# Optimization experiments

Hardware: AMD Instinct MI355X
Metric: run time of the kernel (lower is better)

## Reference

```python
import jax, jax.numpy as jnp
import numpy as np

B, T, D = 4, 2048, 1024
H = 16
HD = D // H  # 64


def setup_inputs() -> dict:
    key = jax.random.key(0)
    ks = jax.random.split(key, 9)
    x = jax.random.normal(ks[0], (B, T, D), dtype=jnp.float32)
    s = 0.02
    Wq = jax.random.normal(ks[1], (D, D), dtype=jnp.float32) * s
    bq = jnp.zeros((D,), dtype=jnp.float32)
    Wk = jax.random.normal(ks[2], (D, D), dtype=jnp.float32) * s
    bk = jnp.zeros((D,), dtype=jnp.float32)
    Wv = jax.random.normal(ks[3], (D, D), dtype=jnp.float32) * s
    bv = jnp.zeros((D,), dtype=jnp.float32)
    Wo = jax.random.normal(ks[4], (D, D), dtype=jnp.float32) * s
    bo = jnp.zeros((D,), dtype=jnp.float32)
    return {"x": x, "Wq": Wq, "bq": bq, "Wk": Wk, "bk": bk,
            "Wv": Wv, "bv": bv, "Wo": Wo, "bo": bo}


def reference(x, Wq, bq, Wk, bk, Wv, bv, Wo, bo):
    Bn, Tn, Dn = x.shape
    # projections -> [B, H, T, HD]
    def split_heads(y):
        return y.reshape(Bn, Tn, H, HD).transpose(0, 2, 1, 3)
    Q = split_heads(x @ Wq + bq)
    K = split_heads(x @ Wk + bk)
    V = split_heads(x @ Wv + bv)
    scores = jnp.einsum('bhqd,bhkd->bhqk', Q, K) / jnp.sqrt(jnp.float32(HD))
    attn = jax.nn.softmax(scores, axis=-1)           # [B, H, T, T]
    attn_weights = attn.mean(axis=1)                 # [B, T, T] (head-averaged)
    out = jnp.einsum('bhqk,bhkd->bhqd', attn, V)     # [B, H, T, HD]
    out = out.transpose(0, 2, 1, 3).reshape(Bn, Tn, Dn)
    out = out @ Wo + bo                              # [B, T, D]
    # pooling weight: mean over query dim -> [B, 1, T] -> transpose -> [B, T, 1]
    pool_w = attn_weights.mean(axis=1, keepdims=True).transpose(0, 2, 1)
    pooled = (out * pool_w).sum(axis=1)              # [B, D]
    return pooled
```

## Files before the change

kernel.cpp:

```cpp
#include <hip/hip_runtime.h>
#include <hip/hip_bf16.h>
#include <stdint.h>

#define B_ 4
#define T_ 2048
#define D_ 1024
#define H_ 16
#define HD_ 64

#define QSCALE 0.1803368801111244f

typedef __bf16 bf16_t;
typedef __bf16 bf16x8 __attribute__((ext_vector_type(8)));
typedef __bf16 bf16x4 __attribute__((ext_vector_type(4)));
typedef float f32x4 __attribute__((ext_vector_type(4)));

__device__ __forceinline__ f32x4 mfma16(bf16x8 a, bf16x8 b, f32x4 c) {
  return __builtin_amdgcn_mfma_f32_16x16x32_bf16(a, b, c, 0, 0, 0);
}

__device__ __forceinline__ void gload_lds16(const bf16_t* g, bf16_t* l) {
  __builtin_amdgcn_global_load_lds(
      (const __attribute__((address_space(1))) unsigned int*)g,
      (__attribute__((address_space(3))) unsigned int*)l, 16, 0, 0);
}

__device__ __forceinline__ float exp2g(float x) {
  return __builtin_amdgcn_exp2f(x);
}

__global__ __launch_bounds__(256) void conv_x(const float* __restrict__ x,
                                              bf16_t* __restrict__ xb) {
  size_t i = ((size_t)blockIdx.x * 256 + threadIdx.x) * 8;
  float4 a = *(const float4*)(x + i);
  float4 b = *(const float4*)(x + i + 4);
  bf16x8 v;
  v[0] = (bf16_t)a.x; v[1] = (bf16_t)a.y; v[2] = (bf16_t)a.z; v[3] = (bf16_t)a.w;
  v[4] = (bf16_t)b.x; v[5] = (bf16_t)b.y; v[6] = (bf16_t)b.z; v[7] = (bf16_t)b.w;
  *(bf16x8*)(xb + i) = v;
}

__global__ __launch_bounds__(256) void conv_wt3(
    const float* __restrict__ Wq, const float* __restrict__ Wk,
    const float* __restrict__ Wv, bf16_t* __restrict__ WtAll) {
  __shared__ float Ls[64][65];
  const int tid = threadIdx.x;
  const int z = blockIdx.z;
  const float* W = (z == 0) ? Wq : (z == 1) ? Wk : Wv;
  bf16_t* Wt = WtAll + (size_t)z * 1024 * D_;
  const int k0 = blockIdx.y * 64, n0 = blockIdx.x * 64;
  const int rr = tid >> 4, cc = (tid & 15) * 4;
#pragma unroll
  for (int it = 0; it < 4; ++it) {
    int r = rr + it * 16;
    float4 v = *(const float4*)(W + (size_t)(k0 + r) * D_ + n0 + cc);
    Ls[r][cc] = v.x; Ls[r][cc + 1] = v.y; Ls[r][cc + 2] = v.z; Ls[r][cc + 3] = v.w;
  }
  __syncthreads();
#pragma unroll
  for (int it = 0; it < 4; ++it) {
    int nl = rr + it * 16;
    bf16x4 o;
    o[0] = (bf16_t)Ls[cc][nl];     o[1] = (bf16_t)Ls[cc + 1][nl];
    o[2] = (bf16_t)Ls[cc + 2][nl]; o[3] = (bf16_t)Ls[cc + 3][nl];
    *(bf16x4*)(Wt + (size_t)(n0 + nl) * D_ + k0 + cc) = o;
  }
}

__global__ __launch_bounds__(256) void gemm_qkv(
    const bf16_t* __restrict__ A, const bf16_t* __restrict__ Bt,
    const float* __restrict__ bq, const float* __restrict__ bk,
    const float* __restrict__ bv,
    bf16_t* __restrict__ Qo, bf16_t* __restrict__ Ko, bf16_t* __restrict__ Vo)
{
  __shared__ __align__(16) bf16_t As[128 * 64];
  __shared__ __align__(16) bf16_t Bs[128 * 64];
  const int tid = threadIdx.x, lane = tid & 63, wv = tid >> 6;
  const int wr = wv >> 1, wc = wv & 1;
  const int wg = blockIdx.x;
  const int xcd = wg & 7;
  const int local = wg >> 3;
  const int mb = xcd * 8 + (local & 7);
  const int nb = local >> 3;
  const int m0 = mb * 128, n0 = nb * 128;
  const int mode = nb >> 3;
  const int lr = lane & 15, lg = lane >> 4;
  const int srow = wv * 8 + (lane >> 3);
  const int scol = (lane & 7) * 8;

  f32x4 acc[4][4] = {};

  for (int k0 = 0; k0 < D_; k0 += 64) {
    __syncthreads();
#pragma unroll
    for (int i = 0; i < 4; ++i) {
      gload_lds16(A + (size_t)(m0 + i * 32 + srow) * D_ + k0 + scol,
                  &As[(i * 32 + wv * 8) * 64]);
      gload_lds16(Bt + (size_t)(n0 + i * 32 + srow) * D_ + k0 + scol,
                  &Bs[(i * 32 + wv * 8) * 64]);
    }
    __syncthreads();

#pragma unroll
    for (int ks = 0; ks < 2; ++ks) {
      bf16x8 af[4], bfr[4];
#pragma unroll
      for (int i = 0; i < 4; ++i)
        af[i] = *(const bf16x8*)&As[(wr * 64 + i * 16 + lr) * 64 + ks * 32 + lg * 8];
#pragma unroll
      for (int j = 0; j < 4; ++j)
        bfr[j] = *(const bf16x8*)&Bs[(wc * 64 + j * 16 + lr) * 64 + ks * 32 + lg * 8];
      if (mode < 2) {
#pragma unroll
        for (int i = 0; i < 4; ++i)
#pragma unroll
          for (int j = 0; j < 4; ++j)
            acc[i][j] = mfma16(af[i], bfr[j], acc[i][j]);
      } else {
#pragma unroll
        for (int i = 0; i < 4; ++i)
#pragma unroll
          for (int j = 0; j < 4; ++j)
            acc[i][j] = mfma16(bfr[j], af[i], acc[i][j]);
      }
    }
  }

  if (mode == 2) {
    const int nl0 = n0 - 2048;
#pragma unroll
    for (int i = 0; i < 4; ++i) {
      int m = m0 + wr * 64 + i * 16 + lr;
      int b = m >> 11, t = m & (T_ - 1);
#pragma unroll
      for (int j = 0; j < 4; ++j)
#pragma unroll
        for (int r = 0; r < 4; ++r) {
          int n = nl0 + wc * 64 + j * 16 + lg * 4 + r;
          int h = n >> 6, d = n & 63;
          float val = acc[i][j][r] + bv[n];
          Vo[((size_t)(b * H_ + h) * HD_ + d) * T_ + t] = (bf16_t)val;
        }
    }
  } else {
    bf16_t* out = mode ? Ko : Qo;
    const float* bias = mode ? bk : bq;
    const float scale = mode ? 1.0f : QSCALE;
    const int nl0 = n0 - mode * 1024;
#pragma unroll
    for (int j = 0; j < 4; ++j) {
      int n = nl0 + wc * 64 + j * 16 + lr;
      float bval = bias[n];
      int h = n >> 6, d = n & 63;
#pragma unroll
      for (int i = 0; i < 4; ++i)
#pragma unroll
        for (int r = 0; r < 4; ++r) {
          int m = m0 + wr * 64 + i * 16 + lg * 4 + r;
          int b = m >> 11, t = m & (T_ - 1);
          float val = (acc[i][j][r] + bval) * scale;
          out[(((size_t)(b * H_ + h)) * T_ + t) * HD_ + d] = (bf16_t)val;
        }
    }
  }
}

template <int OUT_MODE>
__global__ __launch_bounds__(256) void qkv_gemm_f32(
    const float* __restrict__ x, const float* __restrict__ W,
    const float* __restrict__ bias, bf16_t* __restrict__ out, float scale)
{
  __shared__ bf16_t As[128][40];
  __shared__ bf16_t Bs[128][40];
  const int tid = threadIdx.x, lane = tid & 63, wv = tid >> 6;
  const int wr = wv >> 1, wc = wv & 1;
  const int m0 = blockIdx.y * 128, n0 = blockIdx.x * 128;
  const int lr = lane & 15, lg = lane >> 4;
  f32x4 acc[4][4] = {};
  const int xr = tid >> 3, xc = tid & 7;
  const int wk = tid >> 5, wn = tid & 31;

  for (int k0 = 0; k0 < D_; k0 += 32) {
    __syncthreads();
#pragma unroll
    for (int it = 0; it < 4; ++it) {
      int r = xr + it * 32;
      float4 v = *(const float4*)(x + (size_t)(m0 + r) * D_ + k0 + xc * 4);
      bf16_t* dst = &As[r][xc * 4];
      dst[0] = (bf16_t)v.x; dst[1] = (bf16_t)v.y;
      dst[2] = (bf16_t)v.z; dst[3] = (bf16_t)v.w;
    }
#pragma unroll
    for (int it = 0; it < 4; ++it) {
      int k = wk + it * 8;
      float4 v = *(const float4*)(W + (size_t)(k0 + k) * D_ + n0 + wn * 4);
      Bs[wn * 4 + 0][k] = (bf16_t)v.x;
      Bs[wn * 4 + 1][k] = (bf16_t)v.y;
      Bs[wn * 4 + 2][k] = (bf16_t)v.z;
      Bs[wn * 4 + 3][k] = (bf16_t)v.w;
    }
    __syncthreads();
    bf16x8 af[4], bfr[4];
#pragma unroll
    for (int i = 0; i < 4; ++i) af[i]  = *(const bf16x8*)&As[wr * 64 + i * 16 + lr][lg * 8];
#pragma unroll
    for (int j = 0; j < 4; ++j) bfr[j] = *(const bf16x8*)&Bs[wc * 64 + j * 16 + lr][lg * 8];
#pragma unroll
    for (int i = 0; i < 4; ++i)
#pragma unroll
      for (int j = 0; j < 4; ++j) {
        if (OUT_MODE == 0) acc[i][j] = mfma16(af[i], bfr[j], acc[i][j]);
        else               acc[i][j] = mfma16(bfr[j], af[i], acc[i][j]);
      }
  }

  if (OUT_MODE == 0) {
#pragma unroll
    for (int j = 0; j < 4; ++j) {
      int n = n0 + wc * 64 + j * 16 + lr;
      float bval = bias[n];
      int h = n >> 6, d = n & 63;
#pragma unroll
      for (int i = 0; i < 4; ++i)
#pragma unroll
        for (int r = 0; r < 4; ++r) {
          int m = m0 + wr * 64 + i * 16 + lg * 4 + r;
          int b = m >> 11, t = m & (T_ - 1);
          float val = (acc[i][j][r] + bval) * scale;
          out[(((size_t)(b * H_ + h)) * T_ + t) * HD_ + d] = (bf16_t)val;
        }
    }
  } else {
#pragma unroll
    for (int i = 0; i < 4; ++i) {
      int m = m0 + wr * 64 + i * 16 + lr;
      int b = m >> 11, t = m & (T_ - 1);
#pragma unroll
      for (int j = 0; j < 4; ++j)
#pragma unroll
        for (int r = 0; r < 4; ++r) {
          int n = n0 + wc * 64 + j * 16 + lg * 4 + r;
          int h = n >> 6, d = n & 63;
          float val = acc[i][j][r] + bias[n];
          out[((size_t)(b * H_ + h) * HD_ + d) * T_ + t] = (bf16_t)val;
        }
    }
  }
}

__global__ __launch_bounds__(256, 2) void attnA(
    const bf16_t* __restrict__ Q, const bf16_t* __restrict__ K,
    const bf16_t* __restrict__ Vt, bf16_t* __restrict__ O,
    float* __restrict__ Linv)
{
  __shared__ __align__(16) bf16_t Ks[4][64 * 64];
  __shared__ __align__(16) bf16_t Pl[4][2][32 * 64];
  __shared__ float ltab[4][32];

  const int tid = threadIdx.x, lane = tid & 63, wv = tid >> 6;
  const int lr = lane & 15, lg = lane >> 4;
  const int wg = blockIdx.x;
  const int p_ = wg >> 3;
  const int bh = (wg & 7) * 8 + (p_ >> 4);
  const int qb = p_ & 15;
  const int q0 = qb * 128 + wv * 32;
  const int swz = (lr & 7) << 3;
  const int kswz = lr & 7;

  const bf16_t* Qb = Q + (size_t)bh * T_ * HD_;
  const bf16_t* Kb = K + (size_t)bh * T_ * HD_;
  const bf16_t* Vb = Vt + (size_t)bh * HD_ * T_;

  bf16x8 qf0[2], qf1[2];
#pragma unroll
  for (int ks = 0; ks < 2; ++ks) {
    qf0[ks] = *(const bf16x8*)(Qb + (size_t)(q0 + lr) * HD_ + ks * 32 + lg * 8);
    qf1[ks] = *(const bf16x8*)(Qb + (size_t)(q0 + 16 + lr) * HD_ + ks * 32 + lg * 8);
  }

  auto stageK = [&](int buf, int t0) {
    const bf16_t* src = Kb + (size_t)t0 * HD_;
#pragma unroll
    for (int rnd = 0; rnd < 2; ++rnd) {
      const int c = rnd * 256 + tid;
      const int row = c >> 3;
      const int sc16 = (c & 7) ^ (row & 7);
      gload_lds16(src + row * HD_ + sc16 * 8, &Ks[buf][c * 8]);
    }
  };

  float lacc0 = 0.f, lacc1 = 0.f;
  f32x4 oacc[2][4] = {};

  auto computeTile = [&](const bf16_t* Kl, int t0, bf16_t* Pw) {
    bf16x8 vfa[4], vfb[4];
#pragma unroll
    for (int dj = 0; dj < 4; ++dj) {
      vfa[dj] = *(const bf16x8*)(Vb + (size_t)(dj * 16 + lr) * T_ + t0 + lg * 8);
      vfb[dj] = *(const bf16x8*)(Vb + (size_t)(dj * 16 + lr) * T_ + t0 + 32 + lg * 8);
    }
#pragma unroll
    for (int tt = 0; tt < 4; ++tt) {
      const int row = tt * 16 + lr;
      bf16x8 kf0 = *(const bf16x8*)&Kl[row * 64 + ((lg ^ kswz) * 8)];
      bf16x8 kf1 = *(const bf16x8*)&Kl[row * 64 + (((4 + lg) ^ kswz) * 8)];
      f32x4 s0 = {}, s1 = {};
      __builtin_amdgcn_s_setprio(1);
      s0 = mfma16(kf0, qf0[0], s0);
      s0 = mfma16(kf1, qf0[1], s0);
      s1 = mfma16(kf0, qf1[0], s1);
      s1 = mfma16(kf1, qf1[1], s1);
      __builtin_amdgcn_s_setprio(0);
      f32x4 e0, e1;
#pragma unroll
      for (int r = 0; r < 4; ++r) {
        e0[r] = exp2g(s0[r]);
        e1[r] = exp2g(s1[r]);
        lacc0 += e0[r];
        lacc1 += e1[r];
      }
      const int tb = tt * 16 + lg * 4;
      bf16x4 pk0, pk1;
#pragma unroll
      for (int r = 0; r < 4; ++r) { pk0[r] = (bf16_t)e0[r]; pk1[r] = (bf16_t)e1[r]; }
      *(bf16x4*)&Pw[(lr) * 64 + (tb ^ swz)]      = pk0;
      *(bf16x4*)&Pw[(16 + lr) * 64 + (tb ^ swz)] = pk1;
    }

    bf16x8 pf0[2], pf1[2];
#pragma unroll
    for (int ks = 0; ks < 2; ++ks) {
      pf0[ks] = *(const bf16x8*)&Pw[(lr) * 64 + ((ks * 32 + lg * 8) ^ swz)];
      pf1[ks] = *(const bf16x8*)&Pw[(16 + lr) * 64 + ((ks * 32 + lg * 8) ^ swz)];
    }
    __builtin_amdgcn_s_setprio(1);
#pragma unroll
    for (int dj = 0; dj < 4; ++dj) {
      oacc[0][dj] = mfma16(pf0[0], vfa[dj], oacc[0][dj]);
      oacc[0][dj] = mfma16(pf0[1], vfb[dj], oacc[0][dj]);
      oacc[1][dj] = mfma16(pf1[0], vfa[dj], oacc[1][dj]);
      oacc[1][dj] = mfma16(pf1[1], vfb[dj], oacc[1][dj]);
    }
    __builtin_amdgcn_s_setprio(0);
  };

  stageK(0, 0);
  stageK(1, 64);
  __syncthreads();

  for (int p = 0; p < 16; ++p) {
    const int base = (p & 1) ? 2 : 0;
    const int other = base ^ 2;
    if (p < 15) {
      stageK(other,     (2 * p + 2) * 64);
      stageK(other + 1, (2 * p + 3) * 64);
    }
    computeTile(&Ks[base][0],     (2 * p) * 64,     &Pl[wv][0][0]);
    computeTile(&Ks[base + 1][0], (2 * p + 1) * 64, &Pl[wv][1][0]);
    __syncthreads();
  }

  lacc0 += __shfl_xor(lacc0, 16); lacc0 += __shfl_xor(lacc0, 32);
  lacc1 += __shfl_xor(lacc1, 16); lacc1 += __shfl_xor(lacc1, 32);
  const float linv0 = 1.f / lacc0, linv1 = 1.f / lacc1;
  if (lg == 0) {
    ltab[wv][lr] = linv0;
    ltab[wv][16 + lr] = linv1;
    Linv[(size_t)bh * T_ + q0 + lr] = linv0;
    Linv[(size_t)bh * T_ + q0 + 16 + lr] = linv1;
  }
  __syncthreads();

#pragma unroll
  for (int qi = 0; qi < 2; ++qi)
#pragma unroll
    for (int dj = 0; dj < 4; ++dj)
#pragma unroll
      for (int r = 0; r < 4; ++r) {
        int ql = qi * 16 + lg * 4 + r;
        float sc = ltab[wv][ql];
        O[((size_t)bh * T_ + q0 + ql) * HD_ + dj * 16 + lr] =
            (bf16_t)(oacc[qi][dj][r] * sc);
      }
}

__global__ __launch_bounds__(256) void attnB(
    const bf16_t* __restrict__ Q, const bf16_t* __restrict__ K,
    const float* __restrict__ Linv, float* __restrict__ colsum)
{
  const int tid = threadIdx.x, lane = tid & 63, wv = tid >> 6;
  const int lr = lane & 15, lg = lane >> 4;
  const int wg = blockIdx.x;
  const int p_ = wg >> 3;
  const int bh = (wg & 7) * 8 + (p_ >> 4);
  const int rem = p_ & 15;
  const int tc = rem >> 1;
  const int qs = rem & 1;
  const int b = bh >> 4;
  const int t0w = tc * 256 + wv * 64;

  const bf16_t* Qb = Q + (size_t)bh * T_ * HD_;
  const bf16_t* Kb = K + (size_t)bh * T_ * HD_;
  const float* Lb = Linv + (size_t)bh * T_;

  bf16x8 kf[4][2];
#pragma unroll
  for (int tt = 0; tt < 4; ++tt)
#pragma unroll
    for (int ks = 0; ks < 2; ++ks)
      kf[tt][ks] = *(const bf16x8*)(Kb + (size_t)(t0w + tt * 16 + lr) * HD_ +
                                    ks * 32 + lg * 8);

  float acc[4][4] = {};

  const int qlo = qs * (T_ / 2), qhi = qlo + T_ / 2;
  for (int qb = qlo; qb < qhi; qb += 64) {
#pragma unroll
    for (int qt = 0; qt < 4; ++qt) {
      const int q = qb + qt * 16 + lr;
      bf16x8 qv0 = *(const bf16x8*)(Qb + (size_t)q * HD_ + lg * 8);
      bf16x8 qv1 = *(const bf16x8*)(Qb + (size_t)q * HD_ + 32 + lg * 8);
      const float lv = Lb[q];
#pragma unroll
      for (int tt = 0; tt < 4; ++tt) {
        f32x4 s = {};
        __builtin_amdgcn_s_setprio(1);
        s = mfma16(kf[tt][0], qv0, s);
        s = mfma16(kf[tt][1], qv1, s);
        __builtin_amdgcn_s_setprio(0);
#pragma unroll
        for (int r = 0; r < 4; ++r)
          acc[tt][r] = fmaf(exp2g(s[r]), lv, acc[tt][r]);
      }
    }
  }

#pragma unroll
  for (int tt = 0; tt < 4; ++tt)
#pragma unroll
    for (int r = 0; r < 4; ++r) {
      float v = acc[tt][r];
      v += __shfl_xor(v, 1); v += __shfl_xor(v, 2);
      v += __shfl_xor(v, 4); v += __shfl_xor(v, 8);
      acc[tt][r] = v;
    }
  if (lr == 0) {
#pragma unroll
    for (int tt = 0; tt < 4; ++tt)
#pragma unroll
      for (int r = 0; r < 4; ++r)
        atomicAdd(&colsum[b * T_ + t0w + tt * 16 + lg * 4 + r], acc[tt][r]);
  }
}

__global__ __launch_bounds__(256) void pool3(
    const bf16_t* __restrict__ O, const float* __restrict__ CS,
    float* __restrict__ pre)
{
  __shared__ float sm[256];
  const int wg = blockIdx.x;
  const int bh = wg >> 3, tc = wg & 7;
  const int b = bh >> 4, h = bh & 15;
  const int tid = threadIdx.x, d = tid & 63, tg = tid >> 6;
  const bf16_t* Ob = O + (size_t)bh * T_ * HD_ + (size_t)tc * 256 * HD_;
  const float* cw = CS + b * T_ + tc * 256;
  float acc = 0.f;
  for (int t = tg; t < 256; t += 4)
    acc += cw[t] * (float)Ob[(size_t)t * HD_ + d];
  sm[tid] = acc;
  __syncthreads();
  if (tid < 64) {
    float s = sm[tid] + sm[tid + 64] + sm[tid + 128] + sm[tid + 192];
    atomicAdd(&pre[b * D_ + h * 64 + tid], s * (1.f / 32768.f));
  }
}

__global__ __launch_bounds__(256) void out_acc(
    const float* __restrict__ pre, const float* __restrict__ Wo,
    const float* __restrict__ bo, float* __restrict__ out)
{
  const int dc = blockIdx.x & 3, kb = blockIdx.x >> 2;
  const int d = dc * 256 + threadIdx.x;
  const int k0 = kb * 32;
  float acc0 = 0.f, acc1 = 0.f, acc2 = 0.f, acc3 = 0.f;
#pragma unroll
  for (int kk = 0; kk < 32; ++kk) {
    const int k = k0 + kk;
    const float w = Wo[(size_t)k * D_ + d];
    acc0 = fmaf(pre[k],            w, acc0);
    acc1 = fmaf(pre[D_ + k],       w, acc1);
    acc2 = fmaf(pre[2 * D_ + k],   w, acc2);
    acc3 = fmaf(pre[3 * D_ + k],   w, acc3);
  }
  if (kb == 0) {
    const float bd = bo[d];
    acc0 += bd; acc1 += bd; acc2 += bd; acc3 += bd;
  }
  atomicAdd(&out[d],           acc0);
  atomicAdd(&out[D_ + d],      acc1);
  atomicAdd(&out[2 * D_ + d],  acc2);
  atomicAdd(&out[3 * D_ + d],  acc3);
}

extern "C" void kernel_launch(void* const* d_in, const int* in_sizes, int n_in,
                              void* d_out, int out_size, void* d_ws, size_t ws_size,
                              hipStream_t stream)
{
  (void)in_sizes; (void)n_in; (void)out_size;
  const float* x  = (const float*)d_in[0];
  const float* Wq = (const float*)d_in[1];
  const float* bq = (const float*)d_in[2];
  const float* Wk = (const float*)d_in[3];
  const float* bk = (const float*)d_in[4];
  const float* Wv = (const float*)d_in[5];
  const float* bv = (const float*)d_in[6];
  const float* Wo = (const float*)d_in[7];
  const float* bo = (const float*)d_in[8];
  float* out = (float*)d_out;

  char* ws = (char*)d_ws;
  const size_t MB = 1ull << 20;
  bf16_t* Qw  = (bf16_t*)(ws);
  bf16_t* Kw  = (bf16_t*)(ws + 16 * MB);
  bf16_t* Vtw = (bf16_t*)(ws + 32 * MB);
  bf16_t* XO  = (bf16_t*)(ws + 48 * MB);
  const size_t need_fast = 72 * MB;
  const bool fast = ws_size >= need_fast;

  float* LV;
  float* CS;
  float* PRE;
  dim3 blk(256, 1, 1);

  if (fast) {
    bf16_t* WtAll = (bf16_t*)(ws + 64 * MB);
    LV  = (float*)(ws + 70 * MB);
    CS  = (float*)(ws + 70 * MB + 512 * 1024);
    PRE = (float*)(ws + 70 * MB + 512 * 1024 + 32 * 1024);
    conv_x<<<dim3((B_ * T_ * D_) / (256 * 8), 1, 1), blk, 0, stream>>>(x, XO);
    conv_wt3<<<dim3(16, 16, 3), blk, 0, stream>>>(Wq, Wk, Wv, WtAll);
    gemm_qkv<<<dim3(1536, 1, 1), blk, 0, stream>>>(XO, WtAll, bq, bk, bv,
                                                   Qw, Kw, Vtw);
  } else {
    LV  = (float*)(ws + 64 * MB);
    CS  = (float*)(ws + 64 * MB + 512 * 1024);
    PRE = (float*)(ws + 64 * MB + 512 * 1024 + 32 * 1024);
    qkv_gemm_f32<0><<<dim3(8, 64, 1), blk, 0, stream>>>(x, Wq, bq, Qw, QSCALE);
    qkv_gemm_f32<0><<<dim3(8, 64, 1), blk, 0, stream>>>(x, Wk, bk, Kw, 1.0f);
    qkv_gemm_f32<1><<<dim3(8, 64, 1), blk, 0, stream>>>(x, Wv, bv, Vtw, 1.0f);
  }

  hipMemsetAsync(CS, 0, (size_t)(B_ * T_ + B_ * D_) * sizeof(float), stream);
  hipMemsetAsync(out, 0, (size_t)B_ * D_ * sizeof(float), stream);

  attnA<<<dim3(1024, 1, 1), blk, 0, stream>>>(Qw, Kw, Vtw, XO, LV);
  attnB<<<dim3(1024, 1, 1), blk, 0, stream>>>(Qw, Kw, LV, CS);
  pool3<<<dim3(512, 1, 1), blk, 0, stream>>>(XO, CS, PRE);
  out_acc<<<dim3(128, 1, 1), blk, 0, stream>>>(PRE, Wo, bo, out);
}
```

Measured before the change: 306.0 us.

## Reassociate pooling to skip attention output: compute per-key weights then pool V

```diff
diff --git a/kernel.cpp b/kernel.cpp
--- a/kernel.cpp
+++ b/kernel.cpp
@@ -110,62 +110,35 @@
 #pragma unroll
       for (int j = 0; j < 4; ++j)
         bfr[j] = *(const bf16x8*)&Bs[(wc * 64 + j * 16 + lr) * 64 + ks * 32 + lg * 8];
-      if (mode < 2) {
-#pragma unroll
-        for (int i = 0; i < 4; ++i)
-#pragma unroll
-          for (int j = 0; j < 4; ++j)
-            acc[i][j] = mfma16(af[i], bfr[j], acc[i][j]);
-      } else {
-#pragma unroll
-        for (int i = 0; i < 4; ++i)
-#pragma unroll
-          for (int j = 0; j < 4; ++j)
-            acc[i][j] = mfma16(bfr[j], af[i], acc[i][j]);
+#pragma unroll
+      for (int i = 0; i < 4; ++i)
+#pragma unroll
+        for (int j = 0; j < 4; ++j)
+          acc[i][j] = mfma16(af[i], bfr[j], acc[i][j]);
+    }
+  }
+
+  bf16_t* out = (mode == 0) ? Qo : (mode == 1) ? Ko : Vo;
+  const float* bias = (mode == 0) ? bq : (mode == 1) ? bk : bv;
+  const float scale = (mode == 0) ? QSCALE : 1.0f;
+  const int nl0 = n0 - mode * 1024;
+#pragma unroll
+  for (int j = 0; j < 4; ++j) {
+    int n = nl0 + wc * 64 + j * 16 + lr;
+    float bval = bias[n];
+    int h = n >> 6, d = n & 63;
+#pragma unroll
+    for (int i = 0; i < 4; ++i)
+#pragma unroll
+      for (int r = 0; r < 4; ++r) {
+        int m = m0 + wr * 64 + i * 16 + lg * 4 + r;
+        int b = m >> 11, t = m & (T_ - 1);
+        float val = (acc[i][j][r] + bval) * scale;
+        out[(((size_t)(b * H_ + h)) * T_ + t) * HD_ + d] = (bf16_t)val;
       }
-    }
-  }
-
-  if (mode == 2) {
-    const int nl0 = n0 - 2048;
-#pragma unroll
-    for (int i = 0; i < 4; ++i) {
-      int m = m0 + wr * 64 + i * 16 + lr;
-      int b = m >> 11, t = m & (T_ - 1);
-#pragma unroll
-      for (int j = 0; j < 4; ++j)
-#pragma unroll
-        for (int r = 0; r < 4; ++r) {
-          int n = nl0 + wc * 64 + j * 16 + lg * 4 + r;
-          int h = n >> 6, d = n & 63;
-          float val = acc[i][j][r] + bv[n];
-          Vo[((size_t)(b * H_ + h) * HD_ + d) * T_ + t] = (bf16_t)val;
-        }
-    }
-  } else {
-    bf16_t* out = mode ? Ko : Qo;
-    const float* bias = mode ? bk : bq;
-    const float scale = mode ? 1.0f : QSCALE;
-    const int nl0 = n0 - mode * 1024;
-#pragma unroll
-    for (int j = 0; j < 4; ++j) {
-      int n = nl0 + wc * 64 + j * 16 + lr;
-      float bval = bias[n];
-      int h = n >> 6, d = n & 63;
-#pragma unroll
-      for (int i = 0; i < 4; ++i)
-#pragma unroll
-        for (int r = 0; r < 4; ++r) {
-          int m = m0 + wr * 64 + i * 16 + lg * 4 + r;
-          int b = m >> 11, t = m & (T_ - 1);
-          float val = (acc[i][j][r] + bval) * scale;
-          out[(((size_t)(b * H_ + h)) * T_ + t) * HD_ + d] = (bf16_t)val;
-        }
-    }
-  }
-}
-
-template <int OUT_MODE>
+  }
+}
+
 __global__ __launch_bounds__(256) void qkv_gemm_f32(
     const float* __restrict__ x, const float* __restrict__ W,
     const float* __restrict__ bias, bf16_t* __restrict__ out, float scale)
@@ -208,183 +181,92 @@
 #pragma unroll
     for (int i = 0; i < 4; ++i)
 #pragma unroll
-      for (int j = 0; j < 4; ++j) {
-        if (OUT_MODE == 0) acc[i][j] = mfma16(af[i], bfr[j], acc[i][j]);
-        else               acc[i][j] = mfma16(bfr[j], af[i], acc[i][j]);
+      for (int j = 0; j < 4; ++j)
+        acc[i][j] = mfma16(af[i], bfr[j], acc[i][j]);
+  }
+
+#pragma unroll
+  for (int j = 0; j < 4; ++j) {
+    int n = n0 + wc * 64 + j * 16 + lr;
+    float bval = bias[n];
+    int h = n >> 6, d = n & 63;
+#pragma unroll
+    for (int i = 0; i < 4; ++i)
+#pragma unroll
+      for (int r = 0; r < 4; ++r) {
+        int m = m0 + wr * 64 + i * 16 + lg * 4 + r;
+        int b = m >> 11, t = m & (T_ - 1);
+        float val = (acc[i][j][r] + bval) * scale;
+        out[(((size_t)(b * H_ + h)) * T_ + t) * HD_ + d] = (bf16_t)val;
       }
   }
-
-  if (OUT_MODE == 0) {
-#pragma unroll
-    for (int j = 0; j < 4; ++j) {
-      int n = n0 + wc * 64 + j * 16 + lr;
-      float bval = bias[n];
-      int h = n >> 6, d = n & 63;
-#pragma unroll
-      for (int i = 0; i < 4; ++i)
-#pragma unroll
-        for (int r = 0; r < 4; ++r) {
-          int m = m0 + wr * 64 + i * 16 + lg * 4 + r;
-          int b = m >> 11, t = m & (T_ - 1);
-          float val = (acc[i][j][r] + bval) * scale;
-          out[(((size_t)(b * H_ + h)) * T_ + t) * HD_ + d] = (bf16_t)val;
-        }
-    }
-  } else {
-#pragma unroll
-    for (int i = 0; i < 4; ++i) {
-      int m = m0 + wr * 64 + i * 16 + lr;
-      int b = m >> 11, t = m & (T_ - 1);
-#pragma unroll
-      for (int j = 0; j < 4; ++j)
-#pragma unroll
-        for (int r = 0; r < 4; ++r) {
-          int n = n0 + wc * 64 + j * 16 + lg * 4 + r;
-          int h = n >> 6, d = n & 63;
-          float val = acc[i][j][r] + bias[n];
-          out[((size_t)(b * H_ + h) * HD_ + d) * T_ + t] = (bf16_t)val;
-        }
-    }
-  }
-}
-
-__global__ __launch_bounds__(256, 2) void attnA(
+}
+
+__global__ __launch_bounds__(256) void attn_rowsum(
     const bf16_t* __restrict__ Q, const bf16_t* __restrict__ K,
-    const bf16_t* __restrict__ Vt, bf16_t* __restrict__ O,
     float* __restrict__ Linv)
 {
-  __shared__ __align__(16) bf16_t Ks[4][64 * 64];
-  __shared__ __align__(16) bf16_t Pl[4][2][32 * 64];
-  __shared__ float ltab[4][32];
-
   const int tid = threadIdx.x, lane = tid & 63, wv = tid >> 6;
   const int lr = lane & 15, lg = lane >> 4;
   const int wg = blockIdx.x;
   const int p_ = wg >> 3;
   const int bh = (wg & 7) * 8 + (p_ >> 4);
-  const int qb = p_ & 15;
-  const int q0 = qb * 128 + wv * 32;
-  const int swz = (lr & 7) << 3;
-  const int kswz = lr & 7;
+  const int qc = p_ & 15;
+  const int q0w = qc * 128 + wv * 32;
 
   const bf16_t* Qb = Q + (size_t)bh * T_ * HD_;
   const bf16_t* Kb = K + (size_t)bh * T_ * HD_;
-  const bf16_t* Vb = Vt + (size_t)bh * HD_ * T_;
-
-  bf16x8 qf0[2], qf1[2];
-#pragma unroll
-  for (int ks = 0; ks < 2; ++ks) {
-    qf0[ks] = *(const bf16x8*)(Qb + (size_t)(q0 + lr) * HD_ + ks * 32 + lg * 8);
-    qf1[ks] = *(const bf16x8*)(Qb + (size_t)(q0 + 16 + lr) * HD_ + ks * 32 + lg * 8);
-  }
-
-  auto stageK = [&](int buf, int t0) {
-    const bf16_t* src = Kb + (size_t)t0 * HD_;
-#pragma unroll
-    for (int rnd = 0; rnd < 2; ++rnd) {
-      const int c = rnd * 256 + tid;
-      const int row = c >> 3;
-      const int sc16 = (c & 7) ^ (row & 7);
-      gload_lds16(src + row * HD_ + sc16 * 8, &Ks[buf][c * 8]);
-    }
-  };
-
-  float lacc0 = 0.f, lacc1 = 0.f;
-  f32x4 oacc[2][4] = {};
-
-  auto computeTile = [&](const bf16_t* Kl, int t0, bf16_t* Pw) {
-    bf16x8 vfa[4], vfb[4];
-#pragma unroll
-    for (int dj = 0; dj < 4; ++dj) {
-      vfa[dj] = *(const bf16x8*)(Vb + (size_t)(dj * 16 + lr) * T_ + t0 + lg * 8);
-      vfb[dj] = *(const bf16x8*)(Vb + (size_t)(dj * 16 + lr) * T_ + t0 + 32 + lg * 8);
-    }
-#pragma unroll
-    for (int tt = 0; tt < 4; ++tt) {
-      const int row = tt * 16 + lr;
-      bf16x8 kf0 = *(const bf16x8*)&Kl[row * 64 + ((lg ^ kswz) * 8)];
-      bf16x8 kf1 = *(const bf16x8*)&Kl[row * 64 + (((4 + lg) ^ kswz) * 8)];
-      f32x4 s0 = {}, s1 = {};
-      __builtin_amdgcn_s_setprio(1);
-      s0 = mfma16(kf0, qf0[0], s0);
-      s0 = mfma16(kf1, qf0[1], s0);
-      s1 = mfma16(kf0, qf1[0], s1);
-      s1 = mfma16(kf1, qf1[1], s1);
-      __builtin_amdgcn_s_setprio(0);
-      f32x4 e0, e1;
-#pragma unroll
-      for (int r = 0; r < 4; ++r) {
-        e0[r] = exp2g(s0[r]);
-        e1[r] = exp2g(s1[r]);
-        lacc0 += e0[r];
-        lacc1 += e1[r];
+
+  bf16x8 qa[2][2];
+#pragma unroll
+  for (int qq = 0; qq < 2; ++qq)
+#pragma unroll
+    for (int ks = 0; ks < 2; ++ks)
+      qa[qq][ks] = *(const bf16x8*)(Qb + (size_t)(q0w + qq * 16 + lr) * HD_ +
+                                    ks * 32 + lg * 8);
+
+  float accl[2][4] = {};
+
+  for (int tb = 0; tb < T_; tb += 64) {
+#pragma unroll
+    for (int ts = 0; ts < 4; ++ts) {
+      const int t16 = tb + ts * 16;
+      bf16x8 kb0 = *(const bf16x8*)(Kb + (size_t)(t16 + lr) * HD_ + lg * 8);
+      bf16x8 kb1 = *(const bf16x8*)(Kb + (size_t)(t16 + lr) * HD_ + 32 + lg * 8);
+#pragma unroll
+      for (int qq = 0; qq < 2; ++qq) {
+        f32x4 s = {};
+        __builtin_amdgcn_s_setprio(1);
+        s = mfma16(qa[qq][0], kb0, s);
+        s = mfma16(qa[qq][1], kb1, s);
+        __builtin_amdgcn_s_setprio(0);
+#pragma unroll
+        for (int r = 0; r < 4; ++r)
+          accl[qq][r] += exp2g(s[r]);
       }
-      const int tb = tt * 16 + lg * 4;
-      bf16x4 pk0, pk1;
-#pragma unroll
-      for (int r = 0; r < 4; ++r) { pk0[r] = (bf16_t)e0[r]; pk1[r] = (bf16_t)e1[r]; }
-      *(bf16x4*)&Pw[(lr) * 64 + (tb ^ swz)]      = pk0;
-      *(bf16x4*)&Pw[(16 + lr) * 64 + (tb ^ swz)] = pk1;
-    }
-
-    bf16x8 pf0[2], pf1[2];
-#pragma unroll
-    for (int ks = 0; ks < 2; ++ks) {
-      pf0[ks] = *(const bf16x8*)&Pw[(lr) * 64 + ((ks * 32 + lg * 8) ^ swz)];
-      pf1[ks] = *(const bf16x8*)&Pw[(16 + lr) * 64 + ((ks * 32 + lg * 8) ^ swz)];
-    }
-    __builtin_amdgcn_s_setprio(1);
-#pragma unroll
-    for (int dj = 0; dj < 4; ++dj) {
-      oacc[0][dj] = mfma16(pf0[0], vfa[dj], oacc[0][dj]);
-      oacc[0][dj] = mfma16(pf0[1], vfb[dj], oacc[0][dj]);
-      oacc[1][dj] = mfma16(pf1[0], vfa[dj], oacc[1][dj]);
-      oacc[1][dj] = mfma16(pf1[1], vfb[dj], oacc[1][dj]);
-    }
-    __builtin_amdgcn_s_setprio(0);
-  };
-
-  stageK(0, 0);
-  stageK(1, 64);
-  __syncthreads();
-
-  for (int p = 0; p < 16; ++p) {
-    const int base = (p & 1) ? 2 : 0;
-    const int other = base ^ 2;
-    if (p < 15) {
-      stageK(other,     (2 * p + 2) * 64);
-      stageK(other + 1, (2 * p + 3) * 64);
-    }
-    computeTile(&Ks[base][0],     (2 * p) * 64,     &Pl[wv][0][0]);
-    computeTile(&Ks[base + 1][0], (2 * p + 1) * 64, &Pl[wv][1][0]);
-    __syncthreads();
-  }
-
-  lacc0 += __shfl_xor(lacc0, 16); lacc0 += __shfl_xor(lacc0, 32);
-  lacc1 += __shfl_xor(lacc1, 16); lacc1 += __shfl_xor(lacc1, 32);
-  const float linv0 = 1.f / lacc0, linv1 = 1.f / lacc1;
-  if (lg == 0) {
-    ltab[wv][lr] = linv0;
-    ltab[wv][16 + lr] = linv1;
-    Linv[(size_t)bh * T_ + q0 + lr] = linv0;
-    Linv[(size_t)bh * T_ + q0 + 16 + lr] = linv1;
-  }
-  __syncthreads();
-
-#pragma unroll
-  for (int qi = 0; qi < 2; ++qi)
-#pragma unroll
-    for (int dj = 0; dj < 4; ++dj)
-#pragma unroll
-      for (int r = 0; r < 4; ++r) {
-        int ql = qi * 16 + lg * 4 + r;
-        float sc = ltab[wv][ql];
-        O[((size_t)bh * T_ + q0 + ql) * HD_ + dj * 16 + lr] =
-            (bf16_t)(oacc[qi][dj][r] * sc);
-      }
-}
-
-__global__ __launch_bounds__(256) void attnB(
+    }
+  }
+
+#pragma unroll
+  for (int qq = 0; qq < 2; ++qq)
+#pragma unroll
+    for (int r = 0; r < 4; ++r) {
+      float v = accl[qq][r];
+      v += __shfl_xor(v, 1); v += __shfl_xor(v, 2);
+      v += __shfl_xor(v, 4); v += __shfl_xor(v, 8);
+      accl[qq][r] = v;
+    }
+  if (lr == 0) {
+#pragma unroll
+    for (int qq = 0; qq < 2; ++qq)
+#pragma unroll
+      for (int r = 0; r < 4; ++r)
+        Linv[(size_t)bh * T_ + q0w + qq * 16 + lg * 4 + r] =
+            1.f / accl[qq][r];
+  }
+}
+
+__global__ __launch_bounds__(256) void attn_colsum(
     const bf16_t* __restrict__ Q, const bf16_t* __restrict__ K,
     const float* __restrict__ Linv, float* __restrict__ colsum)
 {
@@ -453,25 +335,97 @@
   }
 }
 
-__global__ __launch_bounds__(256) void pool3(
-    const bf16_t* __restrict__ O, const float* __restrict__ CS,
+__global__ __launch_bounds__(256) void attn_w2(
+    const bf16_t* __restrict__ Q, const bf16_t* __restrict__ K,
+    const float* __restrict__ Linv, const float* __restrict__ CS,
+    float* __restrict__ w2)
+{
+  const int tid = threadIdx.x, lane = tid & 63, wv = tid >> 6;
+  const int lr = lane & 15, lg = lane >> 4;
+  const int wg = blockIdx.x;
+  const int p_ = wg >> 3;
+  const int bh = (wg & 7) * 8 + (p_ >> 4);
+  const int rem = p_ & 15;
+  const int tc = rem >> 1;
+  const int qs = rem & 1;
+  const int b = bh >> 4;
+  const int t0w = tc * 256 + wv * 64;
+
+  const bf16_t* Qb = Q + (size_t)bh * T_ * HD_;
+  const bf16_t* Kb = K + (size_t)bh * T_ * HD_;
+  const float* Lb = Linv + (size_t)bh * T_;
+  const float* Cb = CS + (size_t)b * T_;
+
+  bf16x8 kf[4][2];
+#pragma unroll
+  for (int tt = 0; tt < 4; ++tt)
+#pragma unroll
+    for (int ks = 0; ks < 2; ++ks)
+      kf[tt][ks] = *(const bf16x8*)(Kb + (size_t)(t0w + tt * 16 + lr) * HD_ +
+                                    ks * 32 + lg * 8);
+
+  float acc[4][4] = {};
+
+  const int qlo = qs * (T_ / 2), qhi = qlo + T_ / 2;
+  for (int qb = qlo; qb < qhi; qb += 64) {
+#pragma unroll
+    for (int qt = 0; qt < 4; ++qt) {
+      const int q = qb + qt * 16 + lr;
+      bf16x8 qv0 = *(const bf16x8*)(Qb + (size_t)q * HD_ + lg * 8);
+      bf16x8 qv1 = *(const bf16x8*)(Qb + (size_t)q * HD_ + 32 + lg * 8);
+      const float lv = Cb[q] * Lb[q] * (1.f / 32768.f);
+#pragma unroll
+      for (int tt = 0; tt < 4; ++tt) {
+        f32x4 s = {};
+        __builtin_amdgcn_s_setprio(1);
+        s = mfma16(kf[tt][0], qv0, s);
+        s = mfma16(kf[tt][1], qv1, s);
+        __builtin_amdgcn_s_setprio(0);
+#pragma unroll
+        for (int r = 0; r < 4; ++r)
+          acc[tt][r] = fmaf(exp2g(s[r]), lv, acc[tt][r]);
+      }
+    }
+  }
+
+#pragma unroll
+  for (int tt = 0; tt < 4; ++tt)
+#pragma unroll
+    for (int r = 0; r < 4; ++r) {
+      float v = acc[tt][r];
+      v += __shfl_xor(v, 1); v += __shfl_xor(v, 2);
+      v += __shfl_xor(v, 4); v += __shfl_xor(v, 8);
+      acc[tt][r] = v;
+    }
+  if (lr == 0) {
+#pragma unroll
+    for (int tt = 0; tt < 4; ++tt)
+#pragma unroll
+      for (int r = 0; r < 4; ++r)
+        atomicAdd(&w2[(size_t)bh * T_ + t0w + tt * 16 + lg * 4 + r],
+                  acc[tt][r]);
+  }
+}
+
+__global__ __launch_bounds__(256) void pool_wv(
+    const bf16_t* __restrict__ V, const float* __restrict__ W2,
     float* __restrict__ pre)
 {
   __shared__ float sm[256];
   const int wg = blockIdx.x;
-  const int bh = wg >> 3, tc = wg & 7;
+  const int bh = wg >> 3, sc = wg & 7;
   const int b = bh >> 4, h = bh & 15;
   const int tid = threadIdx.x, d = tid & 63, tg = tid >> 6;
-  const bf16_t* Ob = O + (size_t)bh * T_ * HD_ + (size_t)tc * 256 * HD_;
-  const float* cw = CS + b * T_ + tc * 256;
+  const bf16_t* Vb = V + (size_t)bh * T_ * HD_ + (size_t)sc * 256 * HD_;
+  const float* wb = W2 + (size_t)bh * T_ + sc * 256;
   float acc = 0.f;
-  for (int t = tg; t < 256; t += 4)
-    acc += cw[t] * (float)Ob[(size_t)t * HD_ + d];
+  for (int s = tg; s < 256; s += 4)
+    acc += wb[s] * (float)Vb[(size_t)s * HD_ + d];
   sm[tid] = acc;
   __syncthreads();
   if (tid < 64) {
     float s = sm[tid] + sm[tid + 64] + sm[tid + 128] + sm[tid + 192];
-    atomicAdd(&pre[b * D_ + h * 64 + tid], s * (1.f / 32768.f));
+    atomicAdd(&pre[b * D_ + h * 64 + tid], s);
   }
 }
 
@@ -520,41 +474,39 @@
 
   char* ws = (char*)d_ws;
   const size_t MB = 1ull << 20;
-  bf16_t* Qw  = (bf16_t*)(ws);
-  bf16_t* Kw  = (bf16_t*)(ws + 16 * MB);
-  bf16_t* Vtw = (bf16_t*)(ws + 32 * MB);
-  bf16_t* XO  = (bf16_t*)(ws + 48 * MB);
+  const size_t KB = 1024;
+  bf16_t* Qw = (bf16_t*)(ws);
+  bf16_t* Kw = (bf16_t*)(ws + 16 * MB);
+  bf16_t* Vw = (bf16_t*)(ws + 32 * MB);
+  bf16_t* XB = (bf16_t*)(ws + 48 * MB);
   const size_t need_fast = 72 * MB;
   const bool fast = ws_size >= need_fast;
 
-  float* LV;
-  float* CS;
-  float* PRE;
+  size_t soff = fast ? 70 * MB : 64 * MB;
+  float* LV  = (float*)(ws + soff);
+  float* CS  = (float*)(ws + soff + 512 * KB);
+  float* PRE = (float*)(ws + soff + 544 * KB);
+  float* W2  = (float*)(ws + soff + 560 * KB);
   dim3 blk(256, 1, 1);
 
   if (fast) {
     bf16_t* WtAll = (bf16_t*)(ws + 64 * MB);
-    LV  = (float*)(ws + 70 * MB);
-    CS  = (float*)(ws + 70 * MB + 512 * 1024);
-    PRE = (float*)(ws + 70 * MB + 512 * 1024 + 32 * 1024);
-    conv_x<<<dim3((B_ * T_ * D_) / (256 * 8), 1, 1), blk, 0, stream>>>(x, XO);
+    conv_x<<<dim3((B_ * T_ * D_) / (256 * 8), 1, 1), blk, 0, stream>>>(x, XB);
     conv_wt3<<<dim3(16, 16, 3), blk, 0, stream>>>(Wq, Wk, Wv, WtAll);
-    gemm_qkv<<<dim3(1536, 1, 1), blk, 0, stream>>>(XO, WtAll, bq, bk, bv,
-                                                   Qw, Kw, Vtw);
+    gemm_qkv<<<dim3(1536, 1, 1), blk, 0, stream>>>(XB, WtAll, bq, bk, bv,
+                                                   Qw, Kw, Vw);
   } else {
-    LV  = (float*)(ws + 64 * MB);
-    CS  = (float*)(ws + 64 * MB + 512 * 1024);
-    PRE = (float*)(ws + 64 * MB + 512 * 1024 + 32 * 1024);
-    qkv_gemm_f32<0><<<dim3(8, 64, 1), blk, 0, stream>>>(x, Wq, bq, Qw, QSCALE);
-    qkv_gemm_f32<0><<<dim3(8, 64, 1), blk, 0, stream>>>(x, Wk, bk, Kw, 1.0f);
-    qkv_gemm_f32<1><<<dim3(8, 64, 1), blk, 0, stream>>>(x, Wv, bv, Vtw, 1.0f);
-  }
-
-  hipMemsetAsync(CS, 0, (size_t)(B_ * T_ + B_ * D_) * sizeof(float), stream);
+    qkv_gemm_f32<<<dim3(8, 64, 1), blk, 0, stream>>>(x, Wq, bq, Qw, QSCALE);
+    qkv_gemm_f32<<<dim3(8, 64, 1), blk, 0, stream>>>(x, Wk, bk, Kw, 1.0f);
+    qkv_gemm_f32<<<dim3(8, 64, 1), blk, 0, stream>>>(x, Wv, bv, Vw, 1.0f);
+  }
+
+  hipMemsetAsync(CS, 0, 560 * KB - 512 * KB + 512 * KB, stream);
   hipMemsetAsync(out, 0, (size_t)B_ * D_ * sizeof(float), stream);
 
-  attnA<<<dim3(1024, 1, 1), blk, 0, stream>>>(Qw, Kw, Vtw, XO, LV);
-  attnB<<<dim3(1024, 1, 1), blk, 0, stream>>>(Qw, Kw, LV, CS);
-  pool3<<<dim3(512, 1, 1), blk, 0, stream>>>(XO, CS, PRE);
+  attn_rowsum<<<dim3(1024, 1, 1), blk, 0, stream>>>(Qw, Kw, LV);
+  attn_colsum<<<dim3(1024, 1, 1), blk, 0, stream>>>(Qw, Kw, LV, CS);
+  attn_w2<<<dim3(1024, 1, 1), blk, 0, stream>>>(Qw, Kw, LV, CS, W2);
+  pool_wv<<<dim3(512, 1, 1), blk, 0, stream>>>(Vw, W2, PRE);
   out_acc<<<dim3(128, 1, 1), blk, 0, stream>>>(PRE, Wo, bo, out);
 }
```

New measurement: 366.6 us. +19.8%, slower.
